# Optimization experiments

Hardware: AMD Instinct MI355X
Metric: run time of the kernel (lower is better)

The kernel has to match this reference:

```python
import jax, jax.numpy as jnp
import numpy as np

N_EMBED = 768
NUM_EXPERTS = 8
TOP_K = 2
B, S = 2, 2048
THRESH = 1e-09


def setup_inputs() -> dict:
    key = jax.random.key(0)
    ks = jax.random.split(key, 12)
    d, e, f = N_EMBED, NUM_EXPERTS, 4 * N_EMBED
    s_in = 1.0 / np.sqrt(d)
    s_hid = 1.0 / np.sqrt(f)
    return {
        'x': jax.random.normal(ks[0], (B, S, d), jnp.float32),
        'noise': jax.random.normal(ks[1], (B * S, e), jnp.float32),
        'Wg': jax.random.normal(ks[2], (d, e), jnp.float32) * s_in,
        'bg': jnp.zeros((e,), jnp.float32),
        'Wn': jax.random.normal(ks[3], (d, e), jnp.float32) * s_in,
        'bn': jnp.zeros((e,), jnp.float32),
        'W1': jax.random.normal(ks[4], (e, d, f), jnp.float32) * s_in,
        'b1': jnp.zeros((e, f), jnp.float32),
        'W2': jax.random.normal(ks[5], (e, f, d), jnp.float32) * s_hid,
        'b2': jnp.zeros((e, d), jnp.float32),
    }


def reference(x, noise, Wg, bg, Wn, bn, W1, b1, W2, b2):
    Bsz, Ssz, d = x.shape
    T = Bsz * Ssz
    xr = x.reshape(T, d)  # [T, d]

    # Noisy top-k router
    logits = xr @ Wg + bg                     # [T, E]
    noise_logits = xr @ Wn + bn               # [T, E]
    noisy = logits + noise * jax.nn.softplus(noise_logits)
    vals, idx = jax.lax.top_k(noisy, TOP_K)   # [T, K]
    rows = jnp.arange(T)[:, None]
    sparse = jnp.full_like(noisy, -jnp.inf).at[rows, idx].set(vals)
    probs = jax.nn.softmax(sparse, axis=-1)   # [T, E]; zeros off top-k

    # Gate = prob masked by activation threshold (matches torch dispatch)
    gate = jnp.where(probs > THRESH, probs, 0.0)  # [T, E]

    # Dense per-expert MLP (dropout=0 -> identity), combined by gate
    h = jax.nn.relu(jnp.einsum('td,edf->etf', xr, W1) + b1[:, None, :])  # [E, T, 4d]
    y = jnp.einsum('etf,efd->etd', h, W2) + b2[:, None, :]               # [E, T, d]
    out = jnp.einsum('te,etd->td', gate, y)                              # [T, d]
    return out.reshape(Bsz, Ssz, d)
```

## Files before the change

kernel.cpp:

```cpp
#include <hip/hip_runtime.h>
#include <math.h>

typedef unsigned short u16;
typedef unsigned int u32;

#define D_EMB 768
#define F_HID 3072
#define N_TOK 4096
#define N_PAIR 8192
#define GATE_TH 1e-9f

typedef float f32x4 __attribute__((ext_vector_type(4)));
typedef __bf16 bfrag __attribute__((ext_vector_type(8)));

__device__ inline float b2f(u16 u) {
    union { float f; u32 i; } c; c.i = ((u32)u) << 16; return c.f;
}
__device__ inline u16 f2b(float f) {
    union { float f; u32 i; } c; c.f = f;
    u32 r = c.i + 0x7FFFu + ((c.i >> 16) & 1u);
    return (u16)(r >> 16);
}
__device__ inline f32x4 mfma16(bfrag a, bfrag b, f32x4 c) {
    return __builtin_amdgcn_mfma_f32_16x16x32_bf16(a, b, c, 0, 0, 0);
}
__device__ inline void gll16(const u16* g, u16* l) {
    __builtin_amdgcn_global_load_lds(
        (const __attribute__((address_space(1))) u32*)g,
        (__attribute__((address_space(3))) u32*)l, 16, 0, 0);
}
__device__ inline void sbar() {
    asm volatile("" ::: "memory");
    __builtin_amdgcn_s_barrier();
    asm volatile("" ::: "memory");
}
__device__ inline void waitv0() { asm volatile("s_waitcnt vmcnt(0)" ::: "memory"); }
__device__ inline void waitv6() { asm volatile("s_waitcnt vmcnt(6)" ::: "memory"); }
__device__ inline void waitv8() { asm volatile("s_waitcnt vmcnt(8)" ::: "memory"); }

__global__ void moe_init_kernel(int* __restrict__ cnt) {
    if (threadIdx.x < 8) cnt[threadIdx.x] = 0;
}
__global__ __launch_bounds__(256) void moe_zero_kernel(uint4* __restrict__ out) {
    int i = blockIdx.x * 256 + threadIdx.x;
    out[i] = make_uint4(0, 0, 0, 0);
}

__global__ __launch_bounds__(64) void moe_router_v3(
    const float* __restrict__ x, const float* __restrict__ noise,
    const float* __restrict__ Wg, const float* __restrict__ bg,
    const float* __restrict__ Wn, const float* __restrict__ bn,
    int* __restrict__ tk_e, float* __restrict__ tk_g, int* __restrict__ cnt,
    ushort4* __restrict__ xb4)
{
    const int lane = threadIdx.x;
    const int tl = lane & 7, q = lane >> 3;
    const int t = blockIdx.x * 8 + tl;
    float ag[8] = {}, an[8] = {};
    const float4* xp = (const float4*)(x + (size_t)t * D_EMB + q * 96);
#pragma unroll 4
    for (int k4 = 0; k4 < 24; k4++) {
        float4 xv = xp[k4];
        const int kb = q * 96 + k4 * 4;
#pragma unroll
        for (int c = 0; c < 4; c++) {
            float xc = (&xv.x)[c];
            const float4* wg = (const float4*)(Wg + (size_t)(kb + c) * 8);
            const float4* wn = (const float4*)(Wn + (size_t)(kb + c) * 8);
            float4 g0 = wg[0], g1 = wg[1], n0 = wn[0], n1 = wn[1];
            ag[0] += xc * g0.x; ag[1] += xc * g0.y; ag[2] += xc * g0.z; ag[3] += xc * g0.w;
            ag[4] += xc * g1.x; ag[5] += xc * g1.y; ag[6] += xc * g1.z; ag[7] += xc * g1.w;
            an[0] += xc * n0.x; an[1] += xc * n0.y; an[2] += xc * n0.z; an[3] += xc * n0.w;
            an[4] += xc * n1.x; an[5] += xc * n1.y; an[6] += xc * n1.z; an[7] += xc * n1.w;
        }
    }
#pragma unroll
    for (int e = 0; e < 8; e++) {
        ag[e] += __shfl_xor(ag[e], 8);  an[e] += __shfl_xor(an[e], 8);
        ag[e] += __shfl_xor(ag[e], 16); an[e] += __shfl_xor(an[e], 16);
        ag[e] += __shfl_xor(ag[e], 32); an[e] += __shfl_xor(an[e], 32);
    }
    if (q == 0) {
        float best = -INFINITY, sec = -INFINITY; int be = 0, se = 0;
#pragma unroll
        for (int e = 0; e < 8; e++) {
            float nl = an[e] + bn[e];
            float sp = nl > 0.f ? nl + log1pf(expf(-nl)) : log1pf(expf(nl));
            float v = ag[e] + bg[e] + noise[(size_t)t * 8 + e] * sp;
            if (v > best) { sec = best; se = be; best = v; be = e; }
            else if (v > sec) { sec = v; se = e; }
        }
        float ex = expf(sec - best);
        float g1 = 1.f / (1.f + ex), g2 = ex / (1.f + ex);
        tk_e[t * 2 + 0] = (g1 > GATE_TH) ? be : -1; tk_g[t * 2 + 0] = g1;
        tk_e[t * 2 + 1] = (g2 > GATE_TH) ? se : -1; tk_g[t * 2 + 1] = g2;
        if (g1 > GATE_TH) atomicAdd(&cnt[be], 1);
        if (g2 > GATE_TH) atomicAdd(&cnt[se], 1);
    }
    if (xb4) {
        const int t0 = blockIdx.x * 8;
        for (int i = lane; i < 8 * 192; i += 64) {
            int ti = i / 192, c = i - ti * 192;
            float4 v = *(const float4*)(x + (size_t)(t0 + ti) * D_EMB + c * 4);
            ushort4 o;
            o.x = f2b(v.x); o.y = f2b(v.y); o.z = f2b(v.z); o.w = f2b(v.w);
            xb4[(size_t)(t0 + ti) * 192 + c] = o;
        }
    }
}

__global__ void moe_offsets_kernel(const int* __restrict__ cnt,
                                   int* __restrict__ off, int* __restrict__ cursor) {
    if (threadIdx.x == 0) {
        int s = 0;
        for (int e = 0; e < 8; e++) { off[e] = s; cursor[e] = s; s += cnt[e]; }
    }
}
__global__ void moe_scatter_kernel(const int* __restrict__ tk_e, const float* __restrict__ tk_g,
                                   int* __restrict__ cursor, int* __restrict__ plist,
                                   float* __restrict__ pg, int* __restrict__ pos) {
    int i = blockIdx.x * 256 + threadIdx.x;
    if (i < N_PAIR) {
        int e = tk_e[i];
        if (e >= 0) {
            int p = atomicAdd(&cursor[e], 1);
            plist[p] = i >> 1;
            pg[p] = tk_g[i];
            pos[i] = p;
        }
    }
}

__global__ __launch_bounds__(256) void moe_transcvt_kernel(
    const float* __restrict__ in, u16* __restrict__ out, int R, int C) {
    __shared__ float tile[32][33];
    const int z = blockIdx.z;
    const int c0 = blockIdx.x * 32, r0 = blockIdx.y * 32;
    const int tx = threadIdx.x & 31, ty = threadIdx.x >> 5;
    const size_t base = (size_t)z * R * C;
#pragma unroll
    for (int j = 0; j < 32; j += 8)
        tile[ty + j][tx] = in[base + (size_t)(r0 + ty + j) * C + c0 + tx];
    __syncthreads();
    const int c = threadIdx.x >> 3, rb = (threadIdx.x & 7) * 4;
    ushort4 o;
    o.x = f2b(tile[rb + 0][c]);
    o.y = f2b(tile[rb + 1][c]);
    o.z = f2b(tile[rb + 2][c]);
    o.w = f2b(tile[rb + 3][c]);
    *(ushort4*)(out + base + (size_t)(c0 + c) * R + r0 + rb) = o;
}

__global__ __launch_bounds__(256) void moe_ffn1_kernel(
    const u16* __restrict__ xb, const u16* __restrict__ wt, const float* __restrict__ b1,
    const int* __restrict__ plist, const int* __restrict__ cnt, const int* __restrict__ off,
    u16* __restrict__ h, int P0, int P1)
{
    __shared__ __align__(16) u16 As[2][128 * 64];
    __shared__ __align__(16) u16 Bs[2][128 * 64];
    const int GX = 24, GY = 16;
    int f = blockIdx.x + GX * (blockIdx.y + GY * blockIdx.z);
    int swz = (f & 7) * 384 + (f >> 3);
    int nb = swz % GX;
    int t2 = swz / GX;
    int mb = t2 % GY;
    int e  = t2 / GY;

    int lo = off[e], hi = lo + cnt[e];
    if (lo < P0) lo = P0;
    if (hi > P1) hi = P1;
    const int Cl = hi - lo;
    if (Cl <= 0) return;
    const int n0 = nb * 128;
    const int tid = threadIdx.x;
    const int lane = tid & 63, wave = tid >> 6;
    const int wr = wave >> 1, wc = wave & 1;
    const int qq = lane >> 4, r = lane & 15;
    const int srow = tid >> 3;
    const int gq = (tid & 7) ^ (srow & 7);

    const u16* bsrc[4];
#pragma unroll
    for (int j = 0; j < 4; j++)
        bsrc[j] = wt + ((size_t)e * F_HID + n0 + j * 32 + srow) * D_EMB + gq * 8;

    for (int m0 = mb * 128; m0 < Cl; m0 += GY * 128) {
        const u16* asrc[4];
#pragma unroll
        for (int j = 0; j < 4; j++) {
            int mr = m0 + j * 32 + srow;
            if (mr > Cl - 1) mr = Cl - 1;
            asrc[j] = xb + (size_t)plist[lo + mr] * D_EMB + gq * 8;
        }
        f32x4 acc[4][4] = {};

        auto stage = [&](int kt, int buf) {
            const int k0 = kt * 64;
#pragma unroll
            for (int j = 0; j < 4; j++)
                gll16(asrc[j] + k0, &As[buf][j * 2048 + wave * 512]);
#pragma unroll
            for (int j = 0; j < 4; j++)
                gll16(bsrc[j] + k0, &Bs[buf][j * 2048 + wave * 512]);
        };
        auto compute = [&](int buf) {
#pragma unroll
            for (int kk = 0; kk < 2; kk++) {
                bfrag af[4], bf[4];
#pragma unroll
                for (int i = 0; i < 4; i++) {
                    int rowa = wr * 64 + i * 16 + r;
                    int rowb = wc * 64 + i * 16 + r;
                    int slot = ((qq + 4 * kk) ^ (r & 7)) * 8;
                    af[i] = *(const bfrag*)(&As[buf][rowa * 64 + slot]);
                    bf[i] = *(const bfrag*)(&Bs[buf][rowb * 64 + slot]);
                }
#pragma unroll
                for (int mi = 0; mi < 4; mi++)
#pragma unroll
                    for (int ni = 0; ni < 4; ni++)
                        acc[mi][ni] = mfma16(af[mi], bf[ni], acc[mi][ni]);
            }
        };

        waitv0();
        stage(0, 0);
        for (int kt = 0; kt < 11; kt++) {
            stage(kt + 1, (kt + 1) & 1);
            waitv8(); sbar();
            compute(kt & 1);
            sbar();
        }
        waitv0(); sbar();
        compute(1);

#pragma unroll
        for (int mi = 0; mi < 4; mi++)
#pragma unroll
            for (int ni = 0; ni < 4; ni++) {
                int col = n0 + wc * 64 + ni * 16 + r;
                float bias = b1[(size_t)e * F_HID + col];
#pragma unroll
                for (int i = 0; i < 4; i++) {
                    int m = m0 + wr * 64 + mi * 16 + qq * 4 + i;
                    if (m < Cl) {
                        float v = acc[mi][ni][i] + bias;
                        h[(size_t)(lo - P0 + m) * F_HID + col] = f2b(v > 0.f ? v : 0.f);
                    }
                }
            }
    }
}

__global__ __launch_bounds__(256) void moe_ffn2_kernel(
    const u16* __restrict__ h, const u16* __restrict__ wt, const float* __restrict__ b2,
    const int* __restrict__ cnt, const int* __restrict__ off,
    float* __restrict__ y, int P0, int P1)
{
    __shared__ __align__(16) u16 As[2][64 * 64];
    __shared__ __align__(16) u16 Bs[2][128 * 64];
    const int GX = 6, GY = 32;
    int f = blockIdx.x + GX * (blockIdx.y + GY * blockIdx.z);
    int swz = (f & 7) * 192 + (f >> 3);
    int nb = swz % GX;
    int t2 = swz / GX;
    int mb = t2 % GY;
    int e  = t2 / GY;

    int lo = off[e], hi = lo + cnt[e];
    if (lo < P0) lo = P0;
    if (hi > P1) hi = P1;
    const int Cl = hi - lo;
    if (Cl <= 0) return;
    const int n0 = nb * 128;
    const int tid = threadIdx.x;
    const int lane = tid & 63, wave = tid >> 6;
    const int wr = wave >> 1, wc = wave & 1;
    const int qq = lane >> 4, r = lane & 15;
    const int srow = tid >> 3;
    const int gq = (tid & 7) ^ (srow & 7);
    const int hcap = P1 - P0;

    const u16* bsrc[4];
#pragma unroll
    for (int j = 0; j < 4; j++)
        bsrc[j] = wt + ((size_t)e * D_EMB + n0 + j * 32 + srow) * F_HID + gq * 8;

    for (int m0 = mb * 64; m0 < Cl; m0 += GY * 64) {
        const u16* asrc[2];
#pragma unroll
        for (int j = 0; j < 2; j++) {
            int mr = m0 + j * 32 + srow;
            if (mr > Cl - 1) mr = Cl - 1;
            asrc[j] = h + (size_t)(lo - P0 + ((mr < hcap) ? mr : hcap - 1)) * F_HID + gq * 8;
        }
        f32x4 acc[2][4] = {};

        auto stage = [&](int kt, int buf) {
            const int k0 = kt * 64;
#pragma unroll
            for (int j = 0; j < 2; j++)
                gll16(asrc[j] + k0, &As[buf][j * 2048 + wave * 512]);
#pragma unroll
            for (int j = 0; j < 4; j++)
                gll16(bsrc[j] + k0, &Bs[buf][j * 2048 + wave * 512]);
        };
        auto compute = [&](int buf) {
#pragma unroll
            for (int kk = 0; kk < 2; kk++) {
                bfrag af[2], bf[4];
#pragma unroll
                for (int i = 0; i < 2; i++) {
                    int rowa = wr * 32 + i * 16 + r;
                    int slot = ((qq + 4 * kk) ^ (r & 7)) * 8;
                    af[i] = *(const bfrag*)(&As[buf][rowa * 64 + slot]);
                }
#pragma unroll
                for (int i = 0; i < 4; i++) {
                    int rowb = wc * 64 + i * 16 + r;
                    int slot = ((qq + 4 * kk) ^ (r & 7)) * 8;
                    bf[i] = *(const bfrag*)(&Bs[buf][rowb * 64 + slot]);
                }
#pragma unroll
                for (int mi = 0; mi < 2; mi++)
#pragma unroll
                    for (int ni = 0; ni < 4; ni++)
                        acc[mi][ni] = mfma16(af[mi], bf[ni], acc[mi][ni]);
            }
        };

        waitv0();
        stage(0, 0);
        for (int kt = 0; kt < 47; kt++) {
            stage(kt + 1, (kt + 1) & 1);
            waitv6(); sbar();
            compute(kt & 1);
            sbar();
        }
        waitv0(); sbar();
        compute(1);

#pragma unroll
        for (int mi = 0; mi < 2; mi++)
#pragma unroll
            for (int ni = 0; ni < 4; ni++) {
                int col = n0 + wc * 64 + ni * 16 + r;
                float bias = b2[(size_t)e * D_EMB + col];
#pragma unroll
                for (int i = 0; i < 4; i++) {
                    int m = m0 + wr * 32 + mi * 16 + qq * 4 + i;
                    if (m < Cl)
                        y[(size_t)(lo + m) * D_EMB + col] = acc[mi][ni][i] + bias;
                }
            }
    }
}

__global__ __launch_bounds__(256) void moe_combine_kernel(
    const float* __restrict__ y, const int* __restrict__ tk_e,
    const float* __restrict__ tk_g, const int* __restrict__ pos,
    float4* __restrict__ out)
{
    int i = blockIdx.x * 256 + threadIdx.x;
    int t = i / 192;
    int c = i - t * 192;
    float4 a = make_float4(0.f, 0.f, 0.f, 0.f);
#pragma unroll
    for (int k = 0; k < 2; k++) {
        int e = tk_e[t * 2 + k];
        if (e >= 0) {
            float g = tk_g[t * 2 + k];
            float4 v = ((const float4*)(y + (size_t)pos[t * 2 + k] * D_EMB))[c];
            a.x += g * v.x; a.y += g * v.y; a.z += g * v.z; a.w += g * v.w;
        }
    }
    out[i] = a;
}

#define XSTR 776
#define HSTR 3080
#define BMF 8
__global__ __launch_bounds__(256) void moe_ffn_fused_f32(
    const float* __restrict__ x,
    const float* __restrict__ w1, const float* __restrict__ b1,
    const float* __restrict__ w2, const float* __restrict__ b2,
    const int* __restrict__ plist, const float* __restrict__ pg,
    const int* __restrict__ cnt, const int* __restrict__ off,
    float* __restrict__ out)
{
    __shared__ __align__(16) u16 xs[BMF * XSTR];
    __shared__ __align__(16) u16 hs[BMF * HSTR];
    const int e = blockIdx.x;
    const int Cl = cnt[e];
    if (Cl <= 0) return;
    const int O = off[e];
    const int tid = threadIdx.x;
    for (int t0 = blockIdx.y * BMF; t0 < Cl; t0 += gridDim.y * BMF) {
        for (int ci = tid; ci < BMF * 192; ci += 256) {
            int row = ci / 192, c = ci - row * 192;
            float4 v = make_float4(0.f, 0.f, 0.f, 0.f);
            if (t0 + row < Cl) {
                int tok = plist[O + t0 + row];
                v = *(const float4*)(x + (size_t)tok * D_EMB + c * 4);
            }
            u16* d = &xs[row * XSTR + c * 4];
            d[0] = f2b(v.x); d[1] = f2b(v.y); d[2] = f2b(v.z); d[3] = f2b(v.w);
        }
        __syncthreads();
        for (int wi = tid; wi < BMF * 768; wi += 256) {
            int row = wi / 768, nc = wi - row * 768;
            int n0 = nc * 4;
            float a0 = 0, a1 = 0, a2 = 0, a3 = 0;
            const float* wp = w1 + (size_t)e * D_EMB * F_HID + n0;
            const u16* xr = &xs[row * XSTR];
            for (int k = 0; k < D_EMB; k++) {
                float4 wv = *(const float4*)(wp + (size_t)k * F_HID);
                float xv = b2f(xr[k]);
                a0 += xv * wv.x; a1 += xv * wv.y; a2 += xv * wv.z; a3 += xv * wv.w;
            }
            const float* bp = b1 + (size_t)e * F_HID + n0;
            u16* hp = &hs[row * HSTR + n0];
            float v;
            v = a0 + bp[0]; hp[0] = f2b(v > 0.f ? v : 0.f);
            v = a1 + bp[1]; hp[1] = f2b(v > 0.f ? v : 0.f);
            v = a2 + bp[2]; hp[2] = f2b(v > 0.f ? v : 0.f);
            v = a3 + bp[3]; hp[3] = f2b(v > 0.f ? v : 0.f);
        }
        __syncthreads();
        for (int wi = tid; wi < BMF * 192; wi += 256) {
            int row = wi / 192, nc = wi - row * 192;
            int n0 = nc * 4;
            float a0 = 0, a1 = 0, a2 = 0, a3 = 0;
            const float* wp = w2 + (size_t)e * F_HID * D_EMB + n0;
            const u16* hr = &hs[row * HSTR];
            for (int k = 0; k < F_HID; k++) {
                float4 wv = *(const float4*)(wp + (size_t)k * D_EMB);
                float hv = b2f(hr[k]);
                a0 += hv * wv.x; a1 += hv * wv.y; a2 += hv * wv.z; a3 += hv * wv.w;
            }
            if (t0 + row < Cl) {
                int p = O + t0 + row;
                int tok = plist[p];
                float g = pg[p];
                const float* bp = b2 + (size_t)e * D_EMB + n0;
                float* op = out + (size_t)tok * D_EMB + n0;
                atomicAdd(&op[0], g * (a0 + bp[0]));
                atomicAdd(&op[1], g * (a1 + bp[1]));
                atomicAdd(&op[2], g * (a2 + bp[2]));
                atomicAdd(&op[3], g * (a3 + bp[3]));
            }
        }
        __syncthreads();
    }
}

extern "C" void kernel_launch(void* const* d_in, const int* in_sizes, int n_in,
                              void* d_out, int out_size, void* d_ws, size_t ws_size,
                              hipStream_t stream) {
    const float* x     = (const float*)d_in[0];
    const float* noise = (const float*)d_in[1];
    const float* Wg    = (const float*)d_in[2];
    const float* bg    = (const float*)d_in[3];
    const float* Wn    = (const float*)d_in[4];
    const float* bn    = (const float*)d_in[5];
    const float* W1    = (const float*)d_in[6];
    const float* b1    = (const float*)d_in[7];
    const float* W2    = (const float*)d_in[8];
    const float* b2    = (const float*)d_in[9];
    float* out = (float*)d_out;

    char* ws = (char*)d_ws;
    int*   cnt    = (int*)(ws + 0);
    int*   off    = (int*)(ws + 256);
    int*   cursor = (int*)(ws + 512);
    int*   tk_e   = (int*)(ws + 1024);
    float* tk_g   = (float*)(ws + 33792);
    int*   plist  = (int*)(ws + 66560);
    float* pg     = (float*)(ws + 99328);
    int*   pos    = (int*)(ws + 132096);
    const size_t SMALL  = 164864;
    const size_t WSZ    = 37748736ull;
    const size_t XB_SZ  = 6291456ull;
    const size_t Y_SZ   = 25165824ull;
    const size_t H_FULL = 50331648ull;

    const size_t NEED_A = SMALL + WSZ + XB_SZ + Y_SZ + H_FULL;

    if (ws_size >= NEED_A) {
        u16*   wt = (u16*)(ws + SMALL);
        u16*   xb = (u16*)(ws + SMALL + WSZ);
        float* y  = (float*)(ws + SMALL + WSZ + XB_SZ);
        u16*   h  = (u16*)(ws + SMALL + WSZ + XB_SZ + Y_SZ);

        moe_init_kernel<<<dim3(1), dim3(64), 0, stream>>>(cnt);
        moe_router_v3<<<dim3(512), dim3(64), 0, stream>>>(
            x, noise, Wg, bg, Wn, bn, tk_e, tk_g, cnt, (ushort4*)xb);
        moe_offsets_kernel<<<dim3(1), dim3(64), 0, stream>>>(cnt, off, cursor);
        moe_scatter_kernel<<<dim3(N_PAIR / 256), dim3(256), 0, stream>>>(
            tk_e, tk_g, cursor, plist, pg, pos);
        moe_transcvt_kernel<<<dim3(F_HID / 32, D_EMB / 32, 8), dim3(256), 0, stream>>>(
            W1, wt, D_EMB, F_HID);
        moe_ffn1_kernel<<<dim3(24, 16, 8), dim3(256), 0, stream>>>(
            xb, wt, b1, plist, cnt, off, h, 0, N_PAIR);
        moe_transcvt_kernel<<<dim3(D_EMB / 32, F_HID / 32, 8), dim3(256), 0, stream>>>(
            W2, wt, F_HID, D_EMB);
        moe_ffn2_kernel<<<dim3(6, 32, 8), dim3(256), 0, stream>>>(
            h, wt, b2, cnt, off, y, 0, N_PAIR);
        moe_combine_kernel<<<dim3(3072), dim3(256), 0, stream>>>(
            y, tk_e, tk_g, pos, (float4*)out);
        (void)in_sizes; (void)n_in; (void)out_size;
        return;
    }

    const size_t B_BASE = SMALL + 2 * WSZ + XB_SZ + Y_SZ;
    int pchunk = 0;
    for (int p = N_PAIR; p >= 512; p >>= 1) {
        if (B_BASE + (size_t)p * F_HID * 2 <= ws_size) { pchunk = p; break; }
    }

    moe_init_kernel<<<dim3(1), dim3(64), 0, stream>>>(cnt);
    moe_router_v3<<<dim3(512), dim3(64), 0, stream>>>(
        x, noise, Wg, bg, Wn, bn, tk_e, tk_g, cnt,
        pchunk > 0 ? (ushort4*)(ws + SMALL + 2 * WSZ) : (ushort4*)0);
    moe_offsets_kernel<<<dim3(1), dim3(64), 0, stream>>>(cnt, off, cursor);
    moe_scatter_kernel<<<dim3(N_PAIR / 256), dim3(256), 0, stream>>>(
        tk_e, tk_g, cursor, plist, pg, pos);

    if (pchunk > 0) {
        u16*   w1t = (u16*)(ws + SMALL);
        u16*   w2t = (u16*)(ws + SMALL + WSZ);
        u16*   xb  = (u16*)(ws + SMALL + 2 * WSZ);
        float* y   = (float*)(ws + SMALL + 2 * WSZ + XB_SZ);
        u16*   h   = (u16*)(ws + B_BASE);
        moe_transcvt_kernel<<<dim3(F_HID / 32, D_EMB / 32, 8), dim3(256), 0, stream>>>(
            W1, w1t, D_EMB, F_HID);
        moe_transcvt_kernel<<<dim3(D_EMB / 32, F_HID / 32, 8), dim3(256), 0, stream>>>(
            W2, w2t, F_HID, D_EMB);
        for (int c = 0; c < N_PAIR / pchunk; c++) {
            int P0 = c * pchunk, P1 = P0 + pchunk;
            moe_ffn1_kernel<<<dim3(24, 16, 8), dim3(256), 0, stream>>>(
                xb, w1t, b1, plist, cnt, off, h, P0, P1);
            moe_ffn2_kernel<<<dim3(6, 32, 8), dim3(256), 0, stream>>>(
                h, w2t, b2, cnt, off, y, P0, P1);
        }
        moe_combine_kernel<<<dim3(3072), dim3(256), 0, stream>>>(
            y, tk_e, tk_g, pos, (float4*)out);
    } else {
        moe_zero_kernel<<<dim3(3072), dim3(256), 0, stream>>>((uint4*)out);
        moe_ffn_fused_f32<<<dim3(8, 192), dim3(256), 0, stream>>>(
            x, W1, b1, W2, b2, plist, pg, cnt, off, out);
    }
    (void)in_sizes; (void)n_in; (void)out_size;
}
```

Measured before the change: 455.5 us.

## Merge routing bookkeeping into one plan kernel and widen weight transpose tiles

The init, offsets and scatter kernels and the router's atomic counters are replaced by a single-block plan kernel. It counts per-thread, per-expert pairs in shared memory, prefix-sums them and writes plist, pg and pos in a deterministic order. This removes three launches and the global atomics. The weight transpose-convert kernel now uses 64x64 tiles with float4 loads and 16-byte bf16 stores, meant to improve memory efficiency on the large W1/W2 conversion. The single-block plan kernel is serial and may be slow on its own, with a 256-step loop per expert.

After: 414.0 us. 1.1x faster.

```diff
diff --git a/kernel.cpp b/kernel.cpp
--- a/kernel.cpp
+++ b/kernel.cpp
@@ -12,6 +12,7 @@
 
 typedef float f32x4 __attribute__((ext_vector_type(4)));
 typedef __bf16 bfrag __attribute__((ext_vector_type(8)));
+typedef u16 u16x8 __attribute__((ext_vector_type(8)));
 
 __device__ inline float b2f(u16 u) {
     union { float f; u32 i; } c; c.i = ((u32)u) << 16; return c.f;
@@ -38,19 +39,16 @@
 __device__ inline void waitv6() { asm volatile("s_waitcnt vmcnt(6)" ::: "memory"); }
 __device__ inline void waitv8() { asm volatile("s_waitcnt vmcnt(8)" ::: "memory"); }
 
-__global__ void moe_init_kernel(int* __restrict__ cnt) {
-    if (threadIdx.x < 8) cnt[threadIdx.x] = 0;
-}
 __global__ __launch_bounds__(256) void moe_zero_kernel(uint4* __restrict__ out) {
     int i = blockIdx.x * 256 + threadIdx.x;
     out[i] = make_uint4(0, 0, 0, 0);
 }
 
-__global__ __launch_bounds__(64) void moe_router_v3(
+__global__ __launch_bounds__(64) void moe_router_v4(
     const float* __restrict__ x, const float* __restrict__ noise,
     const float* __restrict__ Wg, const float* __restrict__ bg,
     const float* __restrict__ Wn, const float* __restrict__ bn,
-    int* __restrict__ tk_e, float* __restrict__ tk_g, int* __restrict__ cnt,
+    int* __restrict__ tk_e, float* __restrict__ tk_g,
     ushort4* __restrict__ xb4)
 {
     const int lane = threadIdx.x;
@@ -94,8 +92,6 @@
         float g1 = 1.f / (1.f + ex), g2 = ex / (1.f + ex);
         tk_e[t * 2 + 0] = (g1 > GATE_TH) ? be : -1; tk_g[t * 2 + 0] = g1;
         tk_e[t * 2 + 1] = (g2 > GATE_TH) ? se : -1; tk_g[t * 2 + 1] = g2;
-        if (g1 > GATE_TH) atomicAdd(&cnt[be], 1);
-        if (g2 > GATE_TH) atomicAdd(&cnt[se], 1);
     }
     if (xb4) {
         const int t0 = blockIdx.x * 8;
@@ -109,46 +105,79 @@
     }
 }
 
-__global__ void moe_offsets_kernel(const int* __restrict__ cnt,
-                                   int* __restrict__ off, int* __restrict__ cursor) {
-    if (threadIdx.x == 0) {
+__global__ __launch_bounds__(256) void moe_plan_kernel(
+    const int* __restrict__ tk_e, const float* __restrict__ tk_g,
+    int* __restrict__ cnt, int* __restrict__ off,
+    int* __restrict__ plist, float* __restrict__ pg, int* __restrict__ pos)
+{
+    __shared__ int lc[8 * 256];
+    __shared__ int ob[8];
+    const int t = threadIdx.x;
+#pragma unroll
+    for (int e = 0; e < 8; e++) lc[e * 256 + t] = 0;
+    __syncthreads();
+    const int i0 = t * 32;
+    for (int j = 0; j < 32; j++) {
+        int e = tk_e[i0 + j];
+        if (e >= 0) lc[e * 256 + t]++;
+    }
+    __syncthreads();
+    if (t < 8) {
         int s = 0;
-        for (int e = 0; e < 8; e++) { off[e] = s; cursor[e] = s; s += cnt[e]; }
-    }
-}
-__global__ void moe_scatter_kernel(const int* __restrict__ tk_e, const float* __restrict__ tk_g,
-                                   int* __restrict__ cursor, int* __restrict__ plist,
-                                   float* __restrict__ pg, int* __restrict__ pos) {
-    int i = blockIdx.x * 256 + threadIdx.x;
-    if (i < N_PAIR) {
-        int e = tk_e[i];
+        for (int u = 0; u < 256; u++) {
+            int v = lc[t * 256 + u]; lc[t * 256 + u] = s; s += v;
+        }
+        ob[t] = s;
+    }
+    __syncthreads();
+    if (t == 0) {
+        int s = 0;
+        for (int e = 0; e < 8; e++) {
+            int v = ob[e]; cnt[e] = v; off[e] = s; ob[e] = s; s += v;
+        }
+    }
+    __syncthreads();
+    for (int j = 0; j < 32; j++) {
+        int e = tk_e[i0 + j];
         if (e >= 0) {
-            int p = atomicAdd(&cursor[e], 1);
-            plist[p] = i >> 1;
-            pg[p] = tk_g[i];
-            pos[i] = p;
+            int p = ob[e] + lc[e * 256 + t]++;
+            plist[p] = (i0 + j) >> 1;
+            pg[p] = tk_g[i0 + j];
+            pos[i0 + j] = p;
         }
     }
 }
 
 __global__ __launch_bounds__(256) void moe_transcvt_kernel(
     const float* __restrict__ in, u16* __restrict__ out, int R, int C) {
-    __shared__ float tile[32][33];
+    __shared__ float tile[64][65];
     const int z = blockIdx.z;
-    const int c0 = blockIdx.x * 32, r0 = blockIdx.y * 32;
-    const int tx = threadIdx.x & 31, ty = threadIdx.x >> 5;
+    const int c0 = blockIdx.x * 64, r0 = blockIdx.y * 64;
     const size_t base = (size_t)z * R * C;
-#pragma unroll
-    for (int j = 0; j < 32; j += 8)
-        tile[ty + j][tx] = in[base + (size_t)(r0 + ty + j) * C + c0 + tx];
+    const int t = threadIdx.x;
+    {
+        const int row = t >> 2, cb = (t & 3) * 16;
+        const float* src = in + base + (size_t)(r0 + row) * C + c0 + cb;
+        float4 v0 = ((const float4*)src)[0];
+        float4 v1 = ((const float4*)src)[1];
+        float4 v2 = ((const float4*)src)[2];
+        float4 v3 = ((const float4*)src)[3];
+        float* d = &tile[row][cb];
+        d[0]  = v0.x; d[1]  = v0.y; d[2]  = v0.z; d[3]  = v0.w;
+        d[4]  = v1.x; d[5]  = v1.y; d[6]  = v1.z; d[7]  = v1.w;
+        d[8]  = v2.x; d[9]  = v2.y; d[10] = v2.z; d[11] = v2.w;
+        d[12] = v3.x; d[13] = v3.y; d[14] = v3.z; d[15] = v3.w;
+    }
     __syncthreads();
-    const int c = threadIdx.x >> 3, rb = (threadIdx.x & 7) * 4;
-    ushort4 o;
-    o.x = f2b(tile[rb + 0][c]);
-    o.y = f2b(tile[rb + 1][c]);
-    o.z = f2b(tile[rb + 2][c]);
-    o.w = f2b(tile[rb + 3][c]);
-    *(ushort4*)(out + base + (size_t)(c0 + c) * R + r0 + rb) = o;
+    const int c = t >> 2, rb = (t & 3) * 16;
+    u16x8 o0, o1;
+#pragma unroll
+    for (int i = 0; i < 8; i++) o0[i] = f2b(tile[rb + i][c]);
+#pragma unroll
+    for (int i = 0; i < 8; i++) o1[i] = f2b(tile[rb + 8 + i][c]);
+    u16* dst = out + base + (size_t)(c0 + c) * R + r0 + rb;
+    *(u16x8*)dst = o0;
+    *(u16x8*)(dst + 8) = o1;
 }
 
 __global__ __launch_bounds__(256) void moe_ffn1_kernel(
@@ -472,7 +501,6 @@
     char* ws = (char*)d_ws;
     int*   cnt    = (int*)(ws + 0);
     int*   off    = (int*)(ws + 256);
-    int*   cursor = (int*)(ws + 512);
     int*   tk_e   = (int*)(ws + 1024);
     float* tk_g   = (float*)(ws + 33792);
     int*   plist  = (int*)(ws + 66560);
@@ -492,17 +520,15 @@
         float* y  = (float*)(ws + SMALL + WSZ + XB_SZ);
         u16*   h  = (u16*)(ws + SMALL + WSZ + XB_SZ + Y_SZ);
 
-        moe_init_kernel<<<dim3(1), dim3(64), 0, stream>>>(cnt);
-        moe_router_v3<<<dim3(512), dim3(64), 0, stream>>>(
-            x, noise, Wg, bg, Wn, bn, tk_e, tk_g, cnt, (ushort4*)xb);
-        moe_offsets_kernel<<<dim3(1), dim3(64), 0, stream>>>(cnt, off, cursor);
-        moe_scatter_kernel<<<dim3(N_PAIR / 256), dim3(256), 0, stream>>>(
-            tk_e, tk_g, cursor, plist, pg, pos);
-        moe_transcvt_kernel<<<dim3(F_HID / 32, D_EMB / 32, 8), dim3(256), 0, stream>>>(
+        moe_router_v4<<<dim3(512), dim3(64), 0, stream>>>(
+            x, noise, Wg, bg, Wn, bn, tk_e, tk_g, (ushort4*)xb);
+        moe_plan_kernel<<<dim3(1), dim3(256), 0, stream>>>(
+            tk_e, tk_g, cnt, off, plist, pg, pos);
+        moe_transcvt_kernel<<<dim3(F_HID / 64, D_EMB / 64, 8), dim3(256), 0, stream>>>(
             W1, wt, D_EMB, F_HID);
         moe_ffn1_kernel<<<dim3(24, 16, 8), dim3(256), 0, stream>>>(
             xb, wt, b1, plist, cnt, off, h, 0, N_PAIR);
-        moe_transcvt_kernel<<<dim3(D_EMB / 32, F_HID / 32, 8), dim3(256), 0, stream>>>(
+        moe_transcvt_kernel<<<dim3(D_EMB / 64, F_HID / 64, 8), dim3(256), 0, stream>>>(
             W2, wt, F_HID, D_EMB);
         moe_ffn2_kernel<<<dim3(6, 32, 8), dim3(256), 0, stream>>>(
             h, wt, b2, cnt, off, y, 0, N_PAIR);
@@ -518,13 +544,11 @@
         if (B_BASE + (size_t)p * F_HID * 2 <= ws_size) { pchunk = p; break; }
     }
 
-    moe_init_kernel<<<dim3(1), dim3(64), 0, stream>>>(cnt);
-    moe_router_v3<<<dim3(512), dim3(64), 0, stream>>>(
-        x, noise, Wg, bg, Wn, bn, tk_e, tk_g, cnt,
+    moe_router_v4<<<dim3(512), dim3(64), 0, stream>>>(
+        x, noise, Wg, bg, Wn, bn, tk_e, tk_g,
         pchunk > 0 ? (ushort4*)(ws + SMALL + 2 * WSZ) : (ushort4*)0);
-    moe_offsets_kernel<<<dim3(1), dim3(64), 0, stream>>>(cnt, off, cursor);
-    moe_scatter_kernel<<<dim3(N_PAIR / 256), dim3(256), 0, stream>>>(
-        tk_e, tk_g, cursor, plist, pg, pos);
+    moe_plan_kernel<<<dim3(1), dim3(256), 0, stream>>>(
+        tk_e, tk_g, cnt, off, plist, pg, pos);
 
     if (pchunk > 0) {
         u16*   w1t = (u16*)(ws + SMALL);
@@ -532,9 +556,9 @@
         u16*   xb  = (u16*)(ws + SMALL + 2 * WSZ);
         float* y   = (float*)(ws + SMALL + 2 * WSZ + XB_SZ);
         u16*   h   = (u16*)(ws + B_BASE);
-        moe_transcvt_kernel<<<dim3(F_HID / 32, D_EMB / 32, 8), dim3(256), 0, stream>>>(
+        moe_transcvt_kernel<<<dim3(F_HID / 64, D_EMB / 64, 8), dim3(256), 0, stream>>>(
             W1, w1t, D_EMB, F_HID);
-        moe_transcvt_kernel<<<dim3(D_EMB / 32, F_HID / 32, 8), dim3(256), 0, stream>>>(
+        moe_transcvt_kernel<<<dim3(D_EMB / 64, F_HID / 64, 8), dim3(256), 0, stream>>>(
             W2, w2t, F_HID, D_EMB);
         for (int c = 0; c < N_PAIR / pchunk; c++) {
             int P0 = c * pchunk, P1 = P0 + pchunk;
```
